# Performance work log

Hardware: AMD Instinct MI355X
Metric: run time of the kernel (lower is better)

Reference implementation:

```python
import jax, jax.numpy as jnp
import numpy as np

N, E, G = 50000, 800000, 512
D_IN, HID, E_DIM = 128, 128, 128
NEG_SLOPE = 0.2


def setup_inputs() -> dict:
    key = jax.random.key(0)
    ks = iter(jax.random.split(key, 40))
    nrm = lambda shape, s: jax.random.normal(next(ks), shape, jnp.float32) * s
    lin = lambda i, o: nrm((i, o), 1.0 / np.sqrt(i))
    inp = {
        "x": jax.random.randint(next(ks), (N, 9), 0, 119),
        "edge_index": jax.random.randint(next(ks), (2, E), 0, N),
        "edge_attr": jax.random.randint(next(ks), (E, 3), 0, 5),
        "batch": jnp.sort(jax.random.randint(next(ks), (N,), 0, G)),
        # OGB-style encoders: sum of per-feature embeddings
        "atom_emb": nrm((9, 128, D_IN), 0.1),
        "bond_emb": nrm((3, 8, E_DIM), 0.1),
        # GATv2 layer 1 (in=D_IN)
        "W1l": lin(D_IN, HID), "b1l": jnp.zeros((HID,), jnp.float32),
        "W1r": lin(D_IN, HID), "b1r": jnp.zeros((HID,), jnp.float32),
        "W1e": lin(E_DIM, HID), "att1": nrm((HID,), 1.0 / np.sqrt(HID)),
        "bias1": jnp.zeros((HID,), jnp.float32),
        # GATv2 layer 2 (in=HID)
        "W2l": lin(HID, HID), "b2l": jnp.zeros((HID,), jnp.float32),
        "W2r": lin(HID, HID), "b2r": jnp.zeros((HID,), jnp.float32),
        "W2e": lin(E_DIM, HID), "att2": nrm((HID,), 1.0 / np.sqrt(HID)),
        "bias2": jnp.zeros((HID,), jnp.float32),
        # readout linear
        "Wout": lin(HID, 1), "bout": jnp.zeros((1,), jnp.float32),
    }
    return inp


def _segment_softmax(scores, seg, n):
    m = jax.ops.segment_max(scores, seg, num_segments=n)
    ex = jnp.exp(scores - m[seg])
    s = jax.ops.segment_sum(ex, seg, num_segments=n)
    return ex / s[seg]


def _add_self_loops(edge_index, edge_attr):
    # PyG add_self_loops with fill_value='mean': loop attr = mean of incoming edge_attr
    dst = edge_index[1]
    cnt = jax.ops.segment_sum(jnp.ones((E,), edge_attr.dtype), dst, num_segments=N)
    mean_attr = jax.ops.segment_sum(edge_attr, dst, num_segments=N) / jnp.maximum(cnt, 1.0)[:, None]
    loop = jnp.arange(N)
    ei = jnp.concatenate([edge_index, jnp.stack([loop, loop])], axis=1)
    ea = jnp.concatenate([edge_attr, mean_attr], axis=0)
    return ei, ea


def _gatv2(h, src, dst, e_emb, Wl, bl, Wr, br, We, att, bias):
    hl = h @ Wl + bl                      # [N, HID] source transform
    hr = h @ Wr + br                      # [N, HID] target transform
    z = jax.nn.leaky_relu(hl[src] + hr[dst] + e_emb @ We, NEG_SLOPE)  # [E', HID]
    alpha = _segment_softmax(z @ att, dst, N)                          # [E']
    out = jax.ops.segment_sum(alpha[:, None] * hl[src], dst, num_segments=N)
    return out + bias


def reference(x, edge_index, edge_attr, batch, atom_emb, bond_emb,
              W1l, b1l, W1r, b1r, W1e, att1, bias1,
              W2l, b2l, W2r, b2r, W2e, att2, bias2, Wout, bout):
    # encoders: sum of per-feature embedding lookups
    h = jnp.sum(atom_emb[jnp.arange(9)[None, :], x], axis=1)        # [N, D_IN]
    ea = jnp.sum(bond_emb[jnp.arange(3)[None, :], edge_attr], axis=1)  # [E, E_DIM]
    ei, ea = _add_self_loops(edge_index, ea)
    src, dst = ei[0], ei[1]
    h = _gatv2(h, src, dst, ea, W1l, b1l, W1r, b1r, W1e, att1, bias1)
    h = jax.nn.relu(h)
    h = _gatv2(h, src, dst, ea, W2l, b2l, W2r, b2r, W2e, att2, bias2)
    # global mean pool over graphs
    cnt = jax.ops.segment_sum(jnp.ones((N,), h.dtype), batch, num_segments=G)
    g = jax.ops.segment_sum(h, batch, num_segments=G) / jnp.maximum(cnt, 1.0)[:, None]
    # dropout is identity in eval mode
    return jax.nn.sigmoid(g @ Wout + bout)                           # [G, 1]
```

## Files before the change

### kernel.cpp

```cpp
#include <hip/hip_runtime.h>
#include <hip/hip_bf16.h>
#include <math.h>


typedef unsigned int uint;

#define THREADS 256
#define LOG2E 1.4426950408889634f
#define NEGM -1e30f
#define SRC_MASK 0x7fffffu

__device__ inline float4 f4add(float4 x, float4 y) {
  return make_float4(x.x + y.x, x.y + y.y, x.z + y.z, x.w + y.w);
}
__device__ inline float4 f4fma(float c, float4 x, float4 y) {
  return make_float4(fmaf(c, x.x, y.x), fmaf(c, x.y, y.y), fmaf(c, x.z, y.z),
                     fmaf(c, x.w, y.w));
}
__device__ inline float4 f4scale(float4 x, float c) {
  return make_float4(x.x * c, x.y * c, x.z * c, x.w * c);
}
__device__ inline float lrelu_dot(float4 z, float4 a) {
  float r = (z.x > 0.f ? z.x : 0.2f * z.x) * a.x;
  r += (z.y > 0.f ? z.y : 0.2f * z.y) * a.y;
  r += (z.z > 0.f ? z.z : 0.2f * z.z) * a.z;
  r += (z.w > 0.f ? z.w : 0.2f * z.w) * a.w;
  return r;
}
__device__ inline float4 f4relu(float4 x) {
  return make_float4(fmaxf(x.x, 0.f), fmaxf(x.y, 0.f), fmaxf(x.z, 0.f), fmaxf(x.w, 0.f));
}

__global__ void atom_kernel(const int* __restrict__ x, const float* __restrict__ atom_emb,
                            float* __restrict__ h, int n) {
  int idx = blockIdx.x * blockDim.x + threadIdx.x;
  int node = idx >> 7, d = idx & 127;
  if (node >= n) return;
  float s = 0.f;
#pragma unroll
  for (int f = 0; f < 9; f++) {
    int v = x[node * 9 + f];
    s += atom_emb[(f * 128 + v) * 128 + d];
  }
  h[idx] = s;
}

__global__ void edge_hist_kernel(const int* __restrict__ ei, const int* __restrict__ ea,
                                 uint* __restrict__ hist, int E_) {
  int e = blockIdx.x * blockDim.x + threadIdx.x;
  if (e >= E_) return;
  int dst = ei[E_ + e];
  int a0 = ea[e * 3 + 0], a1 = ea[e * 3 + 1], a2 = ea[e * 3 + 2];
  atomicAdd(&hist[dst * 24 + a0], 1u);
  atomicAdd(&hist[dst * 24 + 8 + a1], 1u);
  atomicAdd(&hist[dst * 24 + 16 + a2], 1u);
}

__global__ __launch_bounds__(256) void scanA_kernel(const uint* __restrict__ hist,
                                                    uint* __restrict__ off,
                                                    uint* __restrict__ bsum, int n) {
  __shared__ uint sc[256];
  int t = threadIdx.x;
  int base = blockIdx.x * 1024 + t * 4;
  uint v[4];
#pragma unroll
  for (int i = 0; i < 4; i++) {
    uint d = 0;
    int idx = base + i;
    if (idx < n) {
      const uint4* hp = (const uint4*)&hist[idx * 24];
      uint4 h0 = hp[0], h1 = hp[1];
      d = h0.x + h0.y + h0.z + h0.w + h1.x + h1.y + h1.z + h1.w;
    }
    v[i] = d;
  }
  uint s = v[0] + v[1] + v[2] + v[3];
  sc[t] = s;
  __syncthreads();
  for (int o = 1; o < 256; o <<= 1) {
    uint w = (t >= o) ? sc[t - o] : 0u;
    __syncthreads();
    sc[t] += w;
    __syncthreads();
  }
  uint r = sc[t] - s;
#pragma unroll
  for (int i = 0; i < 4; i++) {
    if (base + i < n) off[base + i] = r;
    r += v[i];
  }
  if (t == 255) bsum[blockIdx.x] = sc[t];
}

__global__ __launch_bounds__(256) void scanB_kernel(const uint* __restrict__ bsum,
                                                    uint* __restrict__ bpre, int nb) {
  __shared__ uint sc[256];
  int t = threadIdx.x;
  uint s = (t < nb) ? bsum[t] : 0u;
  sc[t] = s;
  __syncthreads();
  for (int o = 1; o < 256; o <<= 1) {
    uint w = (t >= o) ? sc[t - o] : 0u;
    __syncthreads();
    sc[t] += w;
    __syncthreads();
  }
  if (t < nb) bpre[t] = sc[t] - s;
}

__global__ void scanC_kernel(uint* __restrict__ off, const uint* __restrict__ bpre, int n,
                             int E_) {
  int i = blockIdx.x * blockDim.x + threadIdx.x;
  if (i < n) off[i] += bpre[i >> 10];
  if (i == 0) off[n] = (uint)E_;
}

__global__ void scatter_kernel(const int* __restrict__ ei, const int* __restrict__ ea,
                               const uint* __restrict__ off, uint* __restrict__ fill,
                               uint* __restrict__ sorted, int E_) {
  int e = blockIdx.x * blockDim.x + threadIdx.x;
  if (e >= E_) return;
  int src = ei[e], dst = ei[E_ + e];
  uint pos = off[dst] + atomicAdd(&fill[dst], 1u);
  uint pk = ((uint)src & SRC_MASK) | ((uint)ea[e * 3 + 0] << 23) |
            ((uint)ea[e * 3 + 1] << 26) | ((uint)ea[e * 3 + 2] << 29);
  sorted[pos] = pk;
}

__global__ void table_kernel(const float* __restrict__ bond_emb, const float* __restrict__ W1e,
                             const float* __restrict__ W2e, float* __restrict__ tab1,
                             float* __restrict__ tab2) {
  __shared__ float row[128];
  int b = blockIdx.x;
  int j = (b < 24) ? b : b - 24;
  const float* We = (b < 24) ? W1e : W2e;
  float* tab = (b < 24) ? tab1 : tab2;
  row[threadIdx.x] = bond_emb[j * 128 + threadIdx.x];
  __syncthreads();
  float acc = 0.f;
#pragma unroll 4
  for (int k = 0; k < 128; k++) acc += row[k] * We[k * 128 + threadIdx.x];
  tab[j * 128 + threadIdx.x] = acc;
}

__global__ __launch_bounds__(256) void lin2_kernel(
    const float* __restrict__ h, const float* __restrict__ Wl, const float* __restrict__ bl,
    const float* __restrict__ Wr, const float* __restrict__ br,
    float* __restrict__ hl, float* __restrict__ hr, int n) {
  __shared__ float hs[32][132];
  int r0 = blockIdx.x * 32;
  for (int i = threadIdx.x; i < 32 * 128; i += 256) {
    int r = i >> 7, c = i & 127;
    int gr = r0 + r;
    hs[r][c] = (gr < n) ? h[gr * 128 + c] : 0.f;
  }
  __syncthreads();
  int col = threadIdx.x & 127;
  int half = threadIdx.x >> 7;
  float accl[16], accr[16];
  float bvl = bl[col], bvr = br[col];
#pragma unroll
  for (int i = 0; i < 16; i++) { accl[i] = bvl; accr[i] = bvr; }
  for (int k = 0; k < 128; k += 4) {
    float wl[4], wr[4];
#pragma unroll
    for (int kk = 0; kk < 4; kk++) {
      wl[kk] = Wl[(k + kk) * 128 + col];
      wr[kk] = Wr[(k + kk) * 128 + col];
    }
#pragma unroll
    for (int i = 0; i < 16; i++) {
      float4 hv = *(const float4*)&hs[half * 16 + i][k];
      accl[i] += hv.x * wl[0] + hv.y * wl[1] + hv.z * wl[2] + hv.w * wl[3];
      accr[i] += hv.x * wr[0] + hv.y * wr[1] + hv.z * wr[2] + hv.w * wr[3];
    }
  }
#pragma unroll
  for (int i = 0; i < 16; i++) {
    int gr = r0 + half * 16 + i;
    if (gr < n) {
      hl[gr * 128 + col] = accl[i];
      hr[gr * 128 + col] = accr[i];
    }
  }
}

__global__ __launch_bounds__(256) void attn_kernel(
    const float* __restrict__ hl, const float* __restrict__ hr,
    const uint* __restrict__ off, const uint* __restrict__ sorted,
    const uint* __restrict__ hist, const float* __restrict__ tab,
    const float* __restrict__ att, const float* __restrict__ bias,
    float* __restrict__ out, int n, int do_relu) {
  __shared__ float tabs[24][128];
  for (int i = threadIdx.x; i < 24 * 128; i += 256) tabs[i >> 7][i & 127] = tab[i];
  __syncthreads();
  int wave = threadIdx.x >> 6, lane = threadIdx.x & 63;
  int node = blockIdx.x * 4 + wave;
  if (node >= n) return;
  int g = lane >> 4;
  int dq = (lane & 15) * 8;

  const float* hrp = &hr[(size_t)node * 128 + dq];
  const float* hlp = &hl[(size_t)node * 128 + dq];
  float4 hr0 = *(const float4*)hrp, hr1 = *(const float4*)(hrp + 4);
  float4 hl0 = *(const float4*)hlp, hl1 = *(const float4*)(hlp + 4);
  float4 at0 = f4scale(*(const float4*)&att[dq], LOG2E);
  float4 at1 = f4scale(*(const float4*)&att[dq + 4], LOG2E);

  float4 ep0 = make_float4(0.f, 0.f, 0.f, 0.f), ep1 = ep0;
  uint c = 0;
#pragma unroll
  for (int j = 0; j < 24; j++) {
    uint hc = hist[node * 24 + j];
    if (j < 8) c += hc;
    if (hc) {
      float f = (float)hc;
      ep0 = f4fma(f, *(const float4*)&tabs[j][dq], ep0);
      ep1 = f4fma(f, *(const float4*)&tabs[j][dq + 4], ep1);
    }
  }
  if (c) {
    float ic = 1.f / (float)c;
    ep0 = f4scale(ep0, ic);
    ep1 = f4scale(ep1, ic);
  }

  auto redscore = [&](float4 z0, float4 z1) -> float {
    float p = lrelu_dot(z0, at0) + lrelu_dot(z1, at1);
    p += __shfl_xor(p, 1);
    p += __shfl_xor(p, 2);
    p += __shfl_xor(p, 4);
    p += __shfl_xor(p, 8);
    return p;
  };

  float sself = redscore(f4add(f4add(hl0, hr0), ep0), f4add(f4add(hl1, hr1), ep1));

  float m, s;
  float4 a0, a1;
  if (g == 0) {
    m = sself; s = 1.f; a0 = hl0; a1 = hl1;
  } else {
    m = NEGM; s = 0.f;
    a0 = make_float4(0.f, 0.f, 0.f, 0.f); a1 = a0;
  }

  uint e0 = off[node], e1 = off[node + 1];
  for (uint base = e0; base < e1; base += 8) {
    uint eA = base + (uint)g, eB = eA + 4u;
    uint iA = eA < e1 ? eA : e1 - 1;
    uint iB = eB < e1 ? eB : e1 - 1;
    uint pkA = sorted[iA], pkB = sorted[iB];
    const float* pa = &hl[(size_t)(pkA & SRC_MASK) * 128 + dq];
    const float* pb = &hl[(size_t)(pkB & SRC_MASK) * 128 + dq];
    float4 hA0 = *(const float4*)pa, hA1 = *(const float4*)(pa + 4);
    float4 hB0 = *(const float4*)pb, hB1 = *(const float4*)(pb + 4);
    int a0A = (pkA >> 23) & 7, a1A = (pkA >> 26) & 7, a2A = (pkA >> 29) & 7;
    int a0B = (pkB >> 23) & 7, a1B = (pkB >> 26) & 7, a2B = (pkB >> 29) & 7;
    float4 eA0 = f4add(f4add(*(const float4*)&tabs[a0A][dq], *(const float4*)&tabs[8 + a1A][dq]),
                       *(const float4*)&tabs[16 + a2A][dq]);
    float4 eA1 = f4add(f4add(*(const float4*)&tabs[a0A][dq + 4],
                             *(const float4*)&tabs[8 + a1A][dq + 4]),
                       *(const float4*)&tabs[16 + a2A][dq + 4]);
    float4 eB0 = f4add(f4add(*(const float4*)&tabs[a0B][dq], *(const float4*)&tabs[8 + a1B][dq]),
                       *(const float4*)&tabs[16 + a2B][dq]);
    float4 eB1 = f4add(f4add(*(const float4*)&tabs[a0B][dq + 4],
                             *(const float4*)&tabs[8 + a1B][dq + 4]),
                       *(const float4*)&tabs[16 + a2B][dq + 4]);
    float scA = redscore(f4add(f4add(hA0, hr0), eA0), f4add(f4add(hA1, hr1), eA1));
    float scB = redscore(f4add(f4add(hB0, hr0), eB0), f4add(f4add(hB1, hr1), eB1));
    if (eA >= e1) scA = NEGM;
    if (eB >= e1) scB = NEGM;
    float mn = fmaxf(m, fmaxf(scA, scB));
    float corr = exp2f(m - mn);
    float pA = exp2f(scA - mn), pB = exp2f(scB - mn);
    s = s * corr + pA + pB;
    a0 = f4fma(pA, hA0, f4fma(pB, hB0, f4scale(a0, corr)));
    a1 = f4fma(pA, hA1, f4fma(pB, hB1, f4scale(a1, corr)));
    m = mn;
  }

#pragma unroll
  for (int lvl = 16; lvl <= 32; lvl <<= 1) {
    float om = __shfl_xor(m, lvl);
    float os = __shfl_xor(s, lvl);
    float4 o0 = make_float4(__shfl_xor(a0.x, lvl), __shfl_xor(a0.y, lvl),
                            __shfl_xor(a0.z, lvl), __shfl_xor(a0.w, lvl));
    float4 o1 = make_float4(__shfl_xor(a1.x, lvl), __shfl_xor(a1.y, lvl),
                            __shfl_xor(a1.z, lvl), __shfl_xor(a1.w, lvl));
    float mn = fmaxf(m, om);
    float ca = exp2f(m - mn), cb = exp2f(om - mn);
    s = s * ca + os * cb;
    a0 = f4fma(cb, o0, f4scale(a0, ca));
    a1 = f4fma(cb, o1, f4scale(a1, ca));
    m = mn;
  }

  float inv = 1.f / s;
  float4 b0 = *(const float4*)&bias[dq], b1 = *(const float4*)&bias[dq + 4];
  float4 o0 = f4fma(inv, a0, b0);
  float4 o1 = f4fma(inv, a1, b1);
  if (do_relu) {
    o0 = f4relu(o0);
    o1 = f4relu(o1);
  }
  if (lane < 16) {
    *(float4*)&out[(size_t)node * 128 + dq] = o0;
    *(float4*)&out[(size_t)node * 128 + dq + 4] = o1;
  }
}

#define POOL_CHUNK 128
__global__ void pool_kernel(const float* __restrict__ h, const int* __restrict__ batch,
                            float* __restrict__ pool, uint* __restrict__ cntg, int n) {
  int d = threadIdx.x;
  int i0 = blockIdx.x * POOL_CHUNK;
  if (i0 >= n) return;
  int i1 = min(i0 + POOL_CHUNK, n);
  int g = batch[i0];
  float s = 0.f;
  uint c = 0;
  for (int i = i0; i < i1; i++) {
    int gi = batch[i];
    if (gi != g) {
      atomicAdd(&pool[g * 128 + d], s);
      if (d == 0) atomicAdd(&cntg[g], c);
      g = gi;
      s = 0.f;
      c = 0;
    }
    s += h[i * 128 + d];
    c++;
  }
  atomicAdd(&pool[g * 128 + d], s);
  if (d == 0) atomicAdd(&cntg[g], c);
}

__global__ void out_kernel(const float* __restrict__ pool, const uint* __restrict__ cntg,
                           const float* __restrict__ Wout, const float* __restrict__ bout,
                           float* __restrict__ out, int g_) {
  int wave = threadIdx.x >> 6, lane = threadIdx.x & 63;
  int g = blockIdx.x * 4 + wave;
  if (g >= g_) return;
  int d = lane * 2;
  float2 pv = *(const float2*)&pool[g * 128 + d];
  float2 wv = *(const float2*)&Wout[d];
  float p = pv.x * wv.x + pv.y * wv.y;
#pragma unroll
  for (int o = 32; o > 0; o >>= 1) p += __shfl_xor(p, o);
  if (lane == 0) {
    uint c = cntg[g];
    float cf = (float)(c ? c : 1u);
    float v = p / cf + bout[0];
    out[g] = 1.f / (1.f + expf(-v));
  }
}

extern "C" void kernel_launch(void* const* d_in, const int* in_sizes, int n_in,
                              void* d_out, int out_size, void* d_ws, size_t ws_size,
                              hipStream_t stream) {
  const int* x          = (const int*)d_in[0];
  const int* edge_index = (const int*)d_in[1];
  const int* edge_attr  = (const int*)d_in[2];
  const int* batch      = (const int*)d_in[3];
  const float* atom_emb = (const float*)d_in[4];
  const float* bond_emb = (const float*)d_in[5];
  const float* W1l = (const float*)d_in[6];
  const float* b1l = (const float*)d_in[7];
  const float* W1r = (const float*)d_in[8];
  const float* b1r = (const float*)d_in[9];
  const float* W1e = (const float*)d_in[10];
  const float* att1 = (const float*)d_in[11];
  const float* bias1 = (const float*)d_in[12];
  const float* W2l = (const float*)d_in[13];
  const float* b2l = (const float*)d_in[14];
  const float* W2r = (const float*)d_in[15];
  const float* b2r = (const float*)d_in[16];
  const float* W2e = (const float*)d_in[17];
  const float* att2 = (const float*)d_in[18];
  const float* bias2 = (const float*)d_in[19];
  const float* Wout = (const float*)d_in[20];
  const float* bout = (const float*)d_in[21];
  float* out = (float*)d_out;

  const int N = in_sizes[0] / 9;
  const int E = in_sizes[1] / 2;
  const int G = out_size;
  const int NB = (N + 1023) / 1024;

  char* w = (char*)d_ws;
  auto alloc = [&](size_t bytes) -> char* {
    char* p = w;
    w += (bytes + 255) & ~(size_t)255;
    return p;
  };
  float* h0     = (float*)alloc((size_t)N * 128 * 4);
  float* hl     = (float*)alloc((size_t)N * 128 * 4);
  float* hr     = (float*)alloc((size_t)N * 128 * 4);
  uint* off     = (uint*)alloc((size_t)(N + 1) * 4);
  uint* fill    = (uint*)alloc((size_t)N * 4);
  uint* hist    = (uint*)alloc((size_t)N * 24 * 4);
  uint* sorted  = (uint*)alloc((size_t)E * 4);
  float* tab1   = (float*)alloc(24 * 128 * 4);
  float* tab2   = (float*)alloc(24 * 128 * 4);
  float* pool   = (float*)alloc((size_t)G * 128 * 4);
  uint* cntg    = (uint*)alloc((size_t)G * 4);
  uint* bsum    = (uint*)alloc((size_t)NB * 4);
  uint* bpre    = (uint*)alloc((size_t)NB * 4);

  hipMemsetAsync(fill, 0, (size_t)N * 4, stream);
  hipMemsetAsync(hist, 0, (size_t)N * 24 * 4, stream);
  hipMemsetAsync(pool, 0, (size_t)G * 128 * 4, stream);
  hipMemsetAsync(cntg, 0, (size_t)G * 4, stream);

  table_kernel<<<48, 128, 0, stream>>>(bond_emb, W1e, W2e, tab1, tab2);
  atom_kernel<<<(N * 128 + THREADS - 1) / THREADS, THREADS, 0, stream>>>(x, atom_emb, h0, N);
  edge_hist_kernel<<<(E + THREADS - 1) / THREADS, THREADS, 0, stream>>>(edge_index, edge_attr,
                                                                        hist, E);
  scanA_kernel<<<NB, 256, 0, stream>>>(hist, off, bsum, N);
  scanB_kernel<<<1, 256, 0, stream>>>(bsum, bpre, NB);
  scanC_kernel<<<(N + THREADS - 1) / THREADS, THREADS, 0, stream>>>(off, bpre, N, E);
  scatter_kernel<<<(E + THREADS - 1) / THREADS, THREADS, 0, stream>>>(edge_index, edge_attr, off,
                                                                      fill, sorted, E);
  lin2_kernel<<<(N + 31) / 32, 256, 0, stream>>>(h0, W1l, b1l, W1r, b1r, hl, hr, N);
  attn_kernel<<<(N + 3) / 4, 256, 0, stream>>>(hl, hr, off, sorted, hist, tab1, att1, bias1,
                                               h0, N, 1);
  lin2_kernel<<<(N + 31) / 32, 256, 0, stream>>>(h0, W2l, b2l, W2r, b2r, hl, hr, N);
  attn_kernel<<<(N + 3) / 4, 256, 0, stream>>>(hl, hr, off, sorted, hist, tab2, att2, bias2,
                                               h0, N, 0);
  pool_kernel<<<(N + POOL_CHUNK - 1) / POOL_CHUNK, 128, 0, stream>>>(h0, batch, pool, cntg, N);
  out_kernel<<<(G + 3) / 4, 256, 0, stream>>>(pool, cntg, Wout, bout, out, G);
}
```

Before: 727.7 us.

## Fuse atom embedding lookup into first-layer linear kernel and pad attention table

Removes the standalone atom embedding kernel and computes the per-node embedding sums directly into shared memory inside the first-layer linear transform, so the N x 128 h0 intermediate is never written to or re-read from global memory. The attention kernel's shared bond-table rows are padded to 132 floats, presumably to reduce LDS bank conflicts. The fused kernel's embedding gathers now run serially before the GEMM in each block, which may lengthen that stage.

```diff
diff --git a/kernel.cpp b/kernel.cpp
--- a/kernel.cpp
+++ b/kernel.cpp
@@ -9,6 +9,7 @@
 #define LOG2E 1.4426950408889634f
 #define NEGM -1e30f
 #define SRC_MASK 0x7fffffu
+#define TPAD 132
 
 __device__ inline float4 f4add(float4 x, float4 y) {
   return make_float4(x.x + y.x, x.y + y.y, x.z + y.z, x.w + y.w);
@@ -29,20 +30,6 @@
 }
 __device__ inline float4 f4relu(float4 x) {
   return make_float4(fmaxf(x.x, 0.f), fmaxf(x.y, 0.f), fmaxf(x.z, 0.f), fmaxf(x.w, 0.f));
-}
-
-__global__ void atom_kernel(const int* __restrict__ x, const float* __restrict__ atom_emb,
-                            float* __restrict__ h, int n) {
-  int idx = blockIdx.x * blockDim.x + threadIdx.x;
-  int node = idx >> 7, d = idx & 127;
-  if (node >= n) return;
-  float s = 0.f;
-#pragma unroll
-  for (int f = 0; f < 9; f++) {
-    int v = x[node * 9 + f];
-    s += atom_emb[(f * 128 + v) * 128 + d];
-  }
-  h[idx] = s;
 }
 
 __global__ void edge_hist_kernel(const int* __restrict__ ei, const int* __restrict__ ea,
@@ -143,6 +130,57 @@
   tab[j * 128 + threadIdx.x] = acc;
 }
 
+__global__ __launch_bounds__(256) void lin2_atom_kernel(
+    const int* __restrict__ x, const float* __restrict__ atom_emb,
+    const float* __restrict__ Wl, const float* __restrict__ bl,
+    const float* __restrict__ Wr, const float* __restrict__ br,
+    float* __restrict__ hl, float* __restrict__ hr, int n) {
+  __shared__ float hs[32][132];
+  int r0 = blockIdx.x * 32;
+  int col = threadIdx.x & 127;
+  int half = threadIdx.x >> 7;
+  for (int i = 0; i < 16; i++) {
+    int r = half * 16 + i;
+    int gr = r0 + r;
+    float s = 0.f;
+    if (gr < n) {
+#pragma unroll
+      for (int f = 0; f < 9; f++) {
+        int v = x[gr * 9 + f];
+        s += atom_emb[(f * 128 + v) * 128 + col];
+      }
+    }
+    hs[r][col] = s;
+  }
+  __syncthreads();
+  float accl[16], accr[16];
+  float bvl = bl[col], bvr = br[col];
+#pragma unroll
+  for (int i = 0; i < 16; i++) { accl[i] = bvl; accr[i] = bvr; }
+  for (int k = 0; k < 128; k += 4) {
+    float wl[4], wr[4];
+#pragma unroll
+    for (int kk = 0; kk < 4; kk++) {
+      wl[kk] = Wl[(k + kk) * 128 + col];
+      wr[kk] = Wr[(k + kk) * 128 + col];
+    }
+#pragma unroll
+    for (int i = 0; i < 16; i++) {
+      float4 hv = *(const float4*)&hs[half * 16 + i][k];
+      accl[i] += hv.x * wl[0] + hv.y * wl[1] + hv.z * wl[2] + hv.w * wl[3];
+      accr[i] += hv.x * wr[0] + hv.y * wr[1] + hv.z * wr[2] + hv.w * wr[3];
+    }
+  }
+#pragma unroll
+  for (int i = 0; i < 16; i++) {
+    int gr = r0 + half * 16 + i;
+    if (gr < n) {
+      hl[gr * 128 + col] = accl[i];
+      hr[gr * 128 + col] = accr[i];
+    }
+  }
+}
+
 __global__ __launch_bounds__(256) void lin2_kernel(
     const float* __restrict__ h, const float* __restrict__ Wl, const float* __restrict__ bl,
     const float* __restrict__ Wr, const float* __restrict__ br,
@@ -191,7 +229,7 @@
     const uint* __restrict__ hist, const float* __restrict__ tab,
     const float* __restrict__ att, const float* __restrict__ bias,
     float* __restrict__ out, int n, int do_relu) {
-  __shared__ float tabs[24][128];
+  __shared__ float tabs[24][TPAD];
   for (int i = threadIdx.x; i < 24 * 128; i += 256) tabs[i >> 7][i & 127] = tab[i];
   __syncthreads();
   int wave = threadIdx.x >> 6, lane = threadIdx.x & 63;
@@ -414,7 +452,6 @@
   hipMemsetAsync(cntg, 0, (size_t)G * 4, stream);
 
   table_kernel<<<48, 128, 0, stream>>>(bond_emb, W1e, W2e, tab1, tab2);
-  atom_kernel<<<(N * 128 + THREADS - 1) / THREADS, THREADS, 0, stream>>>(x, atom_emb, h0, N);
   edge_hist_kernel<<<(E + THREADS - 1) / THREADS, THREADS, 0, stream>>>(edge_index, edge_attr,
                                                                         hist, E);
   scanA_kernel<<<NB, 256, 0, stream>>>(hist, off, bsum, N);
@@ -422,7 +459,7 @@
   scanC_kernel<<<(N + THREADS - 1) / THREADS, THREADS, 0, stream>>>(off, bpre, N, E);
   scatter_kernel<<<(E + THREADS - 1) / THREADS, THREADS, 0, stream>>>(edge_index, edge_attr, off,
                                                                       fill, sorted, E);
-  lin2_kernel<<<(N + 31) / 32, 256, 0, stream>>>(h0, W1l, b1l, W1r, b1r, hl, hr, N);
+  lin2_atom_kernel<<<(N + 31) / 32, 256, 0, stream>>>(x, atom_emb, W1l, b1l, W1r, b1r, hl, hr, N);
   attn_kernel<<<(N + 3) / 4, 256, 0, stream>>>(hl, hr, off, sorted, hist, tab1, att1, bias1,
                                                h0, N, 1);
   lin2_kernel<<<(N + 31) / 32, 256, 0, stream>>>(h0, W2l, b2l, W2r, b2r, hl, hr, N);
```

New measurement: 707.5 us. -2.8%, faster.
